# Kernel tuning notes

Measured on AMD Instinct MI355X. Metric: run time of the kernel, lower is better.

Reference implementation:

```python
import jax, jax.numpy as jnp
import numpy as np

B, S, D, K = 8, 4096, 256, 8192
BETA = 0.25


def setup_inputs() -> dict:
    key = jax.random.key(0)
    k1, k2 = jax.random.split(key)
    return {
        "z": jax.random.normal(k1, (B, S, D), dtype=jnp.float32),
        "embed": jax.random.normal(k2, (K, D), dtype=jnp.float32),
    }


def reference(z, embed):
    # Inference-path VQ-EMA forward (EMA buffer updates are a no-grad side
    # effect only active in training mode; excluded from the pure reference).
    num_codes, dim = embed.shape
    z_flat = z.reshape(-1, dim)                      # [N, D]
    # squared-euclidean distances: ||z||^2 - 2 z.e^T + ||e||^2  -> [N, K]
    dist = ((z_flat * z_flat).sum(1, keepdims=True)
            - 2.0 * (z_flat @ embed.T)
            + (embed * embed).sum(1)[None, :])
    idx = jnp.argmin(dist, axis=1)                   # [N]
    z_q = embed[idx].reshape(z.shape)                # gather instead of onehot @ embed
    # commitment loss: beta * mse(stop_grad(z_q), z)
    loss = BETA * jnp.mean(jnp.square(jax.lax.stop_gradient(z_q) - z))
    # straight-through estimator
    z_q_st = z + jax.lax.stop_gradient(z_q - z)
    # perplexity from code usage histogram (scatter-add instead of onehot.mean)
    counts = jnp.zeros((num_codes,), dtype=z.dtype).at[idx].add(1.0)
    avg_probs = counts / idx.shape[0]
    perplexity = jnp.exp(-jnp.sum(avg_probs * jnp.log(avg_probs + 1e-12)))
    return z_q_st, loss, perplexity, idx.reshape(z.shape[:-1])
```

## Files before the change

kernel.cpp:

```cpp
#include <hip/hip_runtime.h>
#include <stdint.h>
#include <math.h>

#define NROWS 32768
#define DIM   256
#define KCODES 8192
#define BETA  0.25f
#define CSPLIT 4
#define RSPLIT 16
#define NELEM 8388608
#define TAU 0.09375f

typedef float f32x4 __attribute__((ext_vector_type(4)));
typedef _Float16 v8h __attribute__((ext_vector_type(8)));
typedef unsigned short us4 __attribute__((ext_vector_type(4)));

__device__ inline unsigned int split1(float x) {
    _Float16 hf = (_Float16)x;
    _Float16 lf = (_Float16)(x - (float)hf);
    unsigned int h = __builtin_bit_cast(unsigned short, hf);
    unsigned int l = __builtin_bit_cast(unsigned short, lf);
    return h | (l << 16);
}

__device__ inline void gload_lds16(const void* g, void* l) {
    __builtin_amdgcn_global_load_lds(
        (const __attribute__((address_space(1))) void*)g,
        (__attribute__((address_space(3))) void*)l,
        16, 0, 0);
}

__device__ inline unsigned int fkey(float f) {
    unsigned int b = __float_as_uint(f);
    return (b & 0x80000000u) ? ~b : (b | 0x80000000u);
}

__global__ void prep_all(const float* __restrict__ z,
                         const float* __restrict__ e,
                         unsigned short* __restrict__ zhi,
                         unsigned short* __restrict__ zlo,
                         unsigned short* __restrict__ ehi,
                         unsigned short* __restrict__ elo,
                         float* __restrict__ enrm,
                         float* __restrict__ counts,
                         float* __restrict__ lossAcc,
                         int* __restrict__ flagcnt) {
    if (blockIdx.x < 8192) {
        int t = blockIdx.x * 256 + threadIdx.x;
        float4 v = reinterpret_cast<const float4*>(z)[t];
        unsigned int p0 = split1(v.x);
        unsigned int p1 = split1(v.y);
        unsigned int p2 = split1(v.z);
        unsigned int p3 = split1(v.w);
        us4 h, l;
        h[0] = (unsigned short)p0; l[0] = (unsigned short)(p0 >> 16);
        h[1] = (unsigned short)p1; l[1] = (unsigned short)(p1 >> 16);
        h[2] = (unsigned short)p2; l[2] = (unsigned short)(p2 >> 16);
        h[3] = (unsigned short)p3; l[3] = (unsigned short)(p3 >> 16);
        reinterpret_cast<us4*>(zhi)[t] = h;
        reinterpret_cast<us4*>(zlo)[t] = l;
    } else {
        int row = blockIdx.x - 8192;
        int d = threadIdx.x;
        float x = e[(size_t)row * DIM + d];
        unsigned int p = split1(x);
        ehi[(size_t)row * DIM + d] = (unsigned short)p;
        elo[(size_t)row * DIM + d] = (unsigned short)(p >> 16);
        float sq = x * x;
        #pragma unroll
        for (int off = 32; off; off >>= 1) sq += __shfl_down(sq, off);
        __shared__ float ps[4];
        if ((threadIdx.x & 63) == 0) ps[threadIdx.x >> 6] = sq;
        __syncthreads();
        if (threadIdx.x == 0) {
            enrm[row] = 0.5f * (ps[0] + ps[1] + ps[2] + ps[3]);
            counts[row] = 0.f;
            if (row == 0) { *lossAcc = 0.f; *flagcnt = 0; }
        }
    }
}

__launch_bounds__(256, 2)
__global__ void gemm_hi(const unsigned short* __restrict__ zhi,
                        const unsigned short* __restrict__ ehi,
                        const float* __restrict__ enrm,
                        float* __restrict__ pval1,
                        int* __restrict__ pcol1,
                        float* __restrict__ pval2) {
    __shared__ __align__(16) unsigned short As[128 * 64];
    __shared__ __align__(16) unsigned short Bs[128 * 64];
    __shared__ float rv[2][128];
    __shared__ int   rc[2][128];
    __shared__ float rv2[2][128];

    const int tid = threadIdx.x;
    const int w = tid >> 6, l = tid & 63;
    const int lx = l & 15, quad = l >> 4;
    const int wm = w >> 1, wn = w & 1;
    const int arow_base = blockIdx.x * 128;
    const int cs = blockIdx.y;
    const int cbase_cs = cs * (KCODES / CSPLIT);

    float runv[16], runv2[16];
    int runc[16];
    #pragma unroll
    for (int s = 0; s < 16; ++s) {
        runv[s] = 3.0e38f; runv2[s] = 3.0e38f; runc[s] = 0x7fffffff;
    }

    const int st_row8 = l >> 3;
    const int st_g = (((l & 7) ^ (l >> 3)) * 8);
    const int fr_lx7 = lx & 7;

    for (int nt = 0; nt < (KCODES / CSPLIT) / 128; ++nt) {
        const int colbase = cbase_cs + nt * 128;
        f32x4 acc[4][4];
        #pragma unroll
        for (int mi = 0; mi < 4; ++mi)
            #pragma unroll
            for (int ni = 0; ni < 4; ++ni) {
                f32x4 zz = {0.f, 0.f, 0.f, 0.f};
                acc[mi][ni] = zz;
            }

        for (int bk = 0; bk < 4; ++bk) {
            const int ao = bk * 64;
            __syncthreads();
            #pragma unroll
            for (int j = 0; j < 4; ++j) {
                const int r = w * 32 + j * 8 + st_row8;
                gload_lds16(zhi + (size_t)(arow_base + r) * DIM + ao + st_g,
                            &As[(w * 32 + j * 8) * 64]);
                gload_lds16(ehi + (size_t)(colbase + r) * DIM + ao + st_g,
                            &Bs[(w * 32 + j * 8) * 64]);
            }
            __syncthreads();

            #pragma unroll
            for (int kc = 0; kc < 2; ++kc) {
                const int gsw = ((kc * 4 + quad) ^ fr_lx7) * 8;
                v8h af[4], bfr[4];
                #pragma unroll
                for (int mi = 0; mi < 4; ++mi)
                    af[mi] = *(const v8h*)&As[(wm * 64 + mi * 16 + lx) * 64 + gsw];
                #pragma unroll
                for (int ni = 0; ni < 4; ++ni)
                    bfr[ni] = *(const v8h*)&Bs[(wn * 64 + ni * 16 + lx) * 64 + gsw];
                #pragma unroll
                for (int mi = 0; mi < 4; ++mi)
                    #pragma unroll
                    for (int ni = 0; ni < 4; ++ni)
                        acc[mi][ni] = __builtin_amdgcn_mfma_f32_16x16x32_f16(
                            af[mi], bfr[ni], acc[mi][ni], 0, 0, 0);
            }
        }

        #pragma unroll
        for (int ni = 0; ni < 4; ++ni) {
            const int col = colbase + wn * 64 + ni * 16 + lx;
            const float es = enrm[col];
            #pragma unroll
            for (int mi = 0; mi < 4; ++mi)
                #pragma unroll
                for (int r = 0; r < 4; ++r) {
                    const int s = mi * 4 + r;
                    float sv = es - acc[mi][ni][r];
                    bool lt = sv < runv[s];
                    runv2[s] = __builtin_amdgcn_fmed3f(sv, runv[s], runv2[s]);
                    runc[s] = lt ? col : runc[s];
                    runv[s] = fminf(runv[s], sv);
                }
        }
    }

    #pragma unroll
    for (int s = 0; s < 16; ++s) {
        float v1 = runv[s], v2 = runv2[s];
        int c1 = runc[s];
        #pragma unroll
        for (int m = 1; m < 16; m <<= 1) {
            float ov1 = __shfl_xor(v1, m);
            int oc1 = __shfl_xor(c1, m);
            float ov2 = __shfl_xor(v2, m);
            float mx = fmaxf(v1, ov1);
            v2 = fminf(fminf(v2, ov2), mx);
            bool take = (ov1 < v1) || (ov1 == v1 && oc1 < c1);
            v1 = take ? ov1 : v1;
            c1 = take ? oc1 : c1;
        }
        if (lx == 0) {
            const int mi = s >> 2, r = s & 3;
            const int rl = wm * 64 + mi * 16 + quad * 4 + r;
            rv[wn][rl] = v1; rc[wn][rl] = c1; rv2[wn][rl] = v2;
        }
    }
    __syncthreads();
    if (tid < 128) {
        float v1 = rv[0][tid], v2 = rv2[0][tid];
        int c1 = rc[0][tid];
        float ov1 = rv[1][tid], ov2 = rv2[1][tid];
        int oc1 = rc[1][tid];
        float mx = fmaxf(v1, ov1);
        v2 = fminf(fminf(v2, ov2), mx);
        bool take = (ov1 < v1) || (ov1 == v1 && oc1 < c1);
        v1 = take ? ov1 : v1;
        c1 = take ? oc1 : c1;
        const size_t row = (size_t)arow_base + tid;
        pval1[row * CSPLIT + cs] = v1;
        pcol1[row * CSPLIT + cs] = c1;
        pval2[row * CSPLIT + cs] = v2;
    }
}

__global__ void merge_flag(const float* __restrict__ pval1,
                           const int* __restrict__ pcol1,
                           const float* __restrict__ pval2,
                           int* __restrict__ colidx,
                           float* __restrict__ out_idx,
                           int* __restrict__ flagcnt,
                           int* __restrict__ flaglist,
                           unsigned long long* __restrict__ rkey) {
    int row = blockIdx.x * blockDim.x + threadIdx.x;
    float v1 = pval1[row * CSPLIT], v2 = pval2[row * CSPLIT];
    int c1 = pcol1[row * CSPLIT];
    #pragma unroll
    for (int cs = 1; cs < CSPLIT; ++cs) {
        float ov1 = pval1[row * CSPLIT + cs], ov2 = pval2[row * CSPLIT + cs];
        int oc1 = pcol1[row * CSPLIT + cs];
        float mx = fmaxf(v1, ov1);
        v2 = fminf(fminf(v2, ov2), mx);
        if (ov1 < v1 || (ov1 == v1 && oc1 < c1)) { v1 = ov1; c1 = oc1; }
    }
    out_idx[row] = (float)c1;
    if (v2 - v1 < TAU) {
        int slot = atomicAdd(flagcnt, 1);
        flaglist[slot] = row;
        rkey[slot] = ~0ull;
        colidx[row] = -(slot + 1);
    } else {
        colidx[row] = c1;
    }
}

__launch_bounds__(256, 2)
__global__ void rescue_gemm(const unsigned short* __restrict__ zhi,
                            const unsigned short* __restrict__ zlo,
                            const unsigned short* __restrict__ ehi,
                            const unsigned short* __restrict__ elo,
                            const float* __restrict__ enrm,
                            const int* __restrict__ flagcnt,
                            const int* __restrict__ flaglist,
                            unsigned long long* __restrict__ rkey) {
    __shared__ __align__(16) unsigned short As[128 * 64];
    __shared__ __align__(16) unsigned short Bs[128 * 64];
    __shared__ float rv[2][128];
    __shared__ int   rc[2][128];

    const int count = *flagcnt;
    const int tid = threadIdx.x;
    const int w = tid >> 6, l = tid & 63;
    const int lx = l & 15, quad = l >> 4;
    const int wm = w >> 1, wn = w & 1;
    const int cs = blockIdx.y;
    const int cbase_cs = cs * (KCODES / RSPLIT);

    const int st_row8 = l >> 3;
    const int st_g = (((l & 7) ^ (l >> 3)) * 8);
    const int fr_lx7 = lx & 7;

    for (int tb = blockIdx.x * 128; tb < count; tb += 32 * 128) {
        int arowj[4];
        #pragma unroll
        for (int j = 0; j < 4; ++j) {
            int li = tb + w * 32 + j * 8 + st_row8;
            arowj[j] = (li < count) ? flaglist[li] : 0;
        }

        float runv[16];
        int runc[16];
        #pragma unroll
        for (int s = 0; s < 16; ++s) { runv[s] = 3.0e38f; runc[s] = 0x7fffffff; }

        for (int nt = 0; nt < (KCODES / RSPLIT) / 128; ++nt) {
            const int colbase = cbase_cs + nt * 128;
            f32x4 acc[4][4];
            #pragma unroll
            for (int mi = 0; mi < 4; ++mi)
                #pragma unroll
                for (int ni = 0; ni < 4; ++ni) {
                    f32x4 zz = {0.f, 0.f, 0.f, 0.f};
                    acc[mi][ni] = zz;
                }

            #pragma unroll
            for (int seg = 0; seg < 3; ++seg) {
                const unsigned short* za = (seg == 2) ? zlo : zhi;
                const unsigned short* eb = (seg == 1) ? elo : ehi;
                for (int bk = 0; bk < 4; ++bk) {
                    const int ao = bk * 64;
                    __syncthreads();
                    #pragma unroll
                    for (int j = 0; j < 4; ++j) {
                        const int r = w * 32 + j * 8 + st_row8;
                        gload_lds16(za + (size_t)arowj[j] * DIM + ao + st_g,
                                    &As[(w * 32 + j * 8) * 64]);
                        gload_lds16(eb + (size_t)(colbase + r) * DIM + ao + st_g,
                                    &Bs[(w * 32 + j * 8) * 64]);
                    }
                    __syncthreads();
                    #pragma unroll
                    for (int kc = 0; kc < 2; ++kc) {
                        const int gsw = ((kc * 4 + quad) ^ fr_lx7) * 8;
                        v8h af[4], bfr[4];
                        #pragma unroll
                        for (int mi = 0; mi < 4; ++mi)
                            af[mi] = *(const v8h*)&As[(wm * 64 + mi * 16 + lx) * 64 + gsw];
                        #pragma unroll
                        for (int ni = 0; ni < 4; ++ni)
                            bfr[ni] = *(const v8h*)&Bs[(wn * 64 + ni * 16 + lx) * 64 + gsw];
                        #pragma unroll
                        for (int mi = 0; mi < 4; ++mi)
                            #pragma unroll
                            for (int ni = 0; ni < 4; ++ni)
                                acc[mi][ni] = __builtin_amdgcn_mfma_f32_16x16x32_f16(
                                    af[mi], bfr[ni], acc[mi][ni], 0, 0, 0);
                    }
                }
            }

            #pragma unroll
            for (int ni = 0; ni < 4; ++ni) {
                const int col = colbase + wn * 64 + ni * 16 + lx;
                const float es = enrm[col];
                #pragma unroll
                for (int mi = 0; mi < 4; ++mi)
                    #pragma unroll
                    for (int r = 0; r < 4; ++r) {
                        float sv = es - acc[mi][ni][r];
                        const int s = mi * 4 + r;
                        if (sv < runv[s]) { runv[s] = sv; runc[s] = col; }
                    }
            }
        }

        #pragma unroll
        for (int s = 0; s < 16; ++s) {
            float v = runv[s]; int c = runc[s];
            #pragma unroll
            for (int m = 1; m < 16; m <<= 1) {
                float ov = __shfl_xor(v, m);
                int oc = __shfl_xor(c, m);
                if (ov < v || (ov == v && oc < c)) { v = ov; c = oc; }
            }
            if (lx == 0) {
                const int mi = s >> 2, r = s & 3;
                const int rl = wm * 64 + mi * 16 + quad * 4 + r;
                rv[wn][rl] = v; rc[wn][rl] = c;
            }
        }
        __syncthreads();
        if (tid < 128) {
            float v0 = rv[0][tid]; int c0 = rc[0][tid];
            float v1 = rv[1][tid]; int c1 = rc[1][tid];
            if (v1 < v0 || (v1 == v0 && c1 < c0)) { v0 = v1; c0 = c1; }
            const int li = tb + tid;
            if (li < count) {
                unsigned long long key =
                    ((unsigned long long)fkey(v0) << 32) | (unsigned int)c0;
                atomicMin(&rkey[li], key);
            }
        }
        __syncthreads();
    }
}

__global__ void fused_out(const int* __restrict__ colidx,
                          const unsigned long long* __restrict__ rkey,
                          const float* __restrict__ z,
                          const float* __restrict__ embed,
                          float* __restrict__ out_zq,
                          float* __restrict__ out_idx,
                          float* __restrict__ counts,
                          float* __restrict__ lossAcc) {
    __shared__ int cidx[16];
    const int tid = threadIdx.x;
    if (tid < 16) {
        const int row = blockIdx.x * 16 + tid;
        int c = colidx[row];
        if (c < 0) {
            c = (int)(unsigned int)(rkey[-c - 1] & 0x1FFFull);
            out_idx[row] = (float)c;
        }
        cidx[tid] = c;
        atomicAdd(&counts[c], 1.0f);
    }
    __syncthreads();
    const int d = tid;
    float ls = 0.f;
    #pragma unroll 4
    for (int i = 0; i < 16; ++i) {
        const int row = blockIdx.x * 16 + i;
        const int c = cidx[i];
        const float zv = z[(size_t)row * DIM + d];
        const float ev = embed[(size_t)c * DIM + d];
        const float diff = ev - zv;
        out_zq[(size_t)row * DIM + d] = zv + diff;
        ls += diff * diff;
    }
    #pragma unroll
    for (int off = 32; off; off >>= 1) ls += __shfl_down(ls, off);
    __shared__ float ps[4];
    if ((tid & 63) == 0) ps[tid >> 6] = ls;
    __syncthreads();
    if (tid == 0) atomicAdd(lossAcc, ps[0] + ps[1] + ps[2] + ps[3]);
}

__global__ void finalize(const float* __restrict__ counts,
                         const float* __restrict__ lossAcc,
                         float* __restrict__ out_loss,
                         float* __restrict__ out_perp) {
    float h = 0.f;
    for (int k = threadIdx.x; k < KCODES; k += 256) {
        float p = counts[k] * (1.0f / (float)NROWS);
        h += p * logf(p + 1e-12f);
    }
    #pragma unroll
    for (int off = 32; off; off >>= 1) h += __shfl_down(h, off);
    __shared__ float ps[4];
    if ((threadIdx.x & 63) == 0) ps[threadIdx.x >> 6] = h;
    __syncthreads();
    if (threadIdx.x == 0) {
        *out_perp = expf(-(ps[0] + ps[1] + ps[2] + ps[3]));
        *out_loss = BETA * lossAcc[0] / (float)NELEM;
    }
}

extern "C" void kernel_launch(void* const* d_in, const int* in_sizes, int n_in,
                              void* d_out, int out_size, void* d_ws, size_t ws_size,
                              hipStream_t stream) {
    const float* z = (const float*)d_in[0];
    const float* embed = (const float*)d_in[1];
    char* ws = (char*)d_ws;

    unsigned short* zhi = (unsigned short*)(ws + 0);
    unsigned short* zlo = (unsigned short*)(ws + 16777216);
    unsigned short* ehi = (unsigned short*)(ws + 33554432);
    unsigned short* elo = (unsigned short*)(ws + 37748736);
    float* enrm    = (float*)(ws + 41943040);
    float* pval1   = (float*)(ws + 41975808);
    int*   pcol1   = (int*)  (ws + 42500096);
    float* pval2   = (float*)(ws + 43024384);
    int*   colidx  = (int*)  (ws + 43548672);
    float* counts  = (float*)(ws + 43679744);
    float* lossAcc = (float*)(ws + 43712512);
    int*   flagcnt = (int*)  (ws + 43712516);
    int*   flaglist = (int*) (ws + 43712520);
    unsigned long long* rkey = (unsigned long long*)(ws + 43843592);

    float* out = (float*)d_out;
    float* out_zq   = out;
    float* out_loss = out + 8388608;
    float* out_perp = out + 8388609;
    float* out_idx  = out + 8388610;

    prep_all<<<16384, 256, 0, stream>>>(z, embed, zhi, zlo, ehi, elo, enrm,
                                        counts, lossAcc, flagcnt);
    gemm_hi<<<dim3(NROWS / 128, CSPLIT), 256, 0, stream>>>(
        zhi, ehi, enrm, pval1, pcol1, pval2);
    merge_flag<<<NROWS / 256, 256, 0, stream>>>(
        pval1, pcol1, pval2, colidx, out_idx, flagcnt, flaglist, rkey);
    rescue_gemm<<<dim3(32, RSPLIT), 256, 0, stream>>>(
        zhi, zlo, ehi, elo, enrm, flagcnt, flaglist, rkey);
    fused_out<<<NROWS / 16, 256, 0, stream>>>(colidx, rkey, z, embed,
                                              out_zq, out_idx, counts, lossAcc);
    finalize<<<1, 256, 0, stream>>>(counts, lossAcc, out_loss, out_perp);
}
```

Measured before the change: 369.3 us.

## Fuse hi-precision GEMM with merge; keep A in registers and ring-buffer B tiles

Replaces the codebook-split GEMM plus separate merge kernel with one 512-thread kernel per 128-row block. Each block scans all 8192 codes, holds the z fragments in registers for the whole run, and keeps code norms in LDS. B tiles stream through a 4-stage LDS ring with async global-to-LDS loads, explicit vmcnt waits and priority hints. The top-2 merge and flagging happen in-kernel, which removes the partial-result buffers and one launch. The trade-off is a grid of only 256 blocks, which may reduce parallelism on the device, plus high register pressure from the 32 A fragments.

```diff
diff --git a/kernel.cpp b/kernel.cpp
--- a/kernel.cpp
+++ b/kernel.cpp
@@ -6,7 +6,6 @@
 #define DIM   256
 #define KCODES 8192
 #define BETA  0.25f
-#define CSPLIT 4
 #define RSPLIT 16
 #define NELEM 8388608
 #define TAU 0.09375f
@@ -80,26 +79,51 @@
     }
 }
 
-__launch_bounds__(256, 2)
-__global__ void gemm_hi(const unsigned short* __restrict__ zhi,
-                        const unsigned short* __restrict__ ehi,
-                        const float* __restrict__ enrm,
-                        float* __restrict__ pval1,
-                        int* __restrict__ pcol1,
-                        float* __restrict__ pval2) {
-    __shared__ __align__(16) unsigned short As[128 * 64];
-    __shared__ __align__(16) unsigned short Bs[128 * 64];
-    __shared__ float rv[2][128];
-    __shared__ int   rc[2][128];
-    __shared__ float rv2[2][128];
+__launch_bounds__(512, 2)
+__global__ void gemm_hi_fused(const unsigned short* __restrict__ zhi,
+                              const unsigned short* __restrict__ ehi,
+                              const float* __restrict__ enrm,
+                              int* __restrict__ colidx,
+                              float* __restrict__ out_idx,
+                              int* __restrict__ flagcnt,
+                              int* __restrict__ flaglist,
+                              unsigned long long* __restrict__ rkey) {
+    __shared__ __align__(16) unsigned short Bs[4][128 * 64];
+    __shared__ float esL[KCODES];
+    __shared__ float rvv[4][128];
+    __shared__ float rv2s[4][128];
+    __shared__ int   rcc[4][128];
 
     const int tid = threadIdx.x;
     const int w = tid >> 6, l = tid & 63;
     const int lx = l & 15, quad = l >> 4;
-    const int wm = w >> 1, wn = w & 1;
+    const int wm = w >> 2, wn = w & 3;
     const int arow_base = blockIdx.x * 128;
-    const int cs = blockIdx.y;
-    const int cbase_cs = cs * (KCODES / CSPLIT);
+    const int st_g = ((l & 7) ^ (l >> 3)) * 8;
+    const int fr_lx7 = lx & 7;
+
+    v8h af[4][8];
+    #pragma unroll
+    for (int mi = 0; mi < 4; ++mi) {
+        const unsigned short* ap =
+            zhi + (size_t)(arow_base + wm * 64 + mi * 16 + lx) * DIM + quad * 8;
+        #pragma unroll
+        for (int ks = 0; ks < 8; ++ks)
+            af[mi][ks] = *(const v8h*)(ap + ks * 32);
+    }
+
+    #pragma unroll
+    for (int j = 0; j < 4; ++j)
+        gload_lds16(enrm + (j * 8 + w) * 256 + l * 4, &esL[(j * 8 + w) * 256]);
+
+#define STAGE(BUF, SN, AO) do {                                               \
+        const unsigned short* _s0 =                                           \
+            ehi + (size_t)((SN) * 128 + (tid >> 3)) * DIM + (AO) + st_g;      \
+        gload_lds16(_s0, &Bs[BUF][(w * 8) * 64]);                             \
+        gload_lds16(_s0 + (size_t)64 * DIM, &Bs[BUF][(64 + w * 8) * 64]);     \
+    } while (0)
+
+    STAGE(0, 0, 0); STAGE(1, 0, 64); STAGE(2, 0, 128);
 
     float runv[16], runv2[16];
     int runc[16];
@@ -108,70 +132,63 @@
         runv[s] = 3.0e38f; runv2[s] = 3.0e38f; runc[s] = 0x7fffffff;
     }
 
-    const int st_row8 = l >> 3;
-    const int st_g = (((l & 7) ^ (l >> 3)) * 8);
-    const int fr_lx7 = lx & 7;
-
-    for (int nt = 0; nt < (KCODES / CSPLIT) / 128; ++nt) {
-        const int colbase = cbase_cs + nt * 128;
-        f32x4 acc[4][4];
+    for (int nt = 0; nt < 64; ++nt) {
+        f32x4 acc[4][2];
         #pragma unroll
         for (int mi = 0; mi < 4; ++mi)
             #pragma unroll
-            for (int ni = 0; ni < 4; ++ni) {
+            for (int ni = 0; ni < 2; ++ni) {
                 f32x4 zz = {0.f, 0.f, 0.f, 0.f};
                 acc[mi][ni] = zz;
             }
 
+        #pragma unroll
         for (int bk = 0; bk < 4; ++bk) {
-            const int ao = bk * 64;
-            __syncthreads();
-            #pragma unroll
-            for (int j = 0; j < 4; ++j) {
-                const int r = w * 32 + j * 8 + st_row8;
-                gload_lds16(zhi + (size_t)(arow_base + r) * DIM + ao + st_g,
-                            &As[(w * 32 + j * 8) * 64]);
-                gload_lds16(ehi + (size_t)(colbase + r) * DIM + ao + st_g,
-                            &Bs[(w * 32 + j * 8) * 64]);
-            }
-            __syncthreads();
-
+            const int sn = (bk == 0) ? nt : ((nt + 1) & 63);
+            STAGE((bk + 3) & 3, sn, ((bk + 3) & 3) * 64);
+            asm volatile("s_waitcnt vmcnt(6)" ::: "memory");
+            __builtin_amdgcn_s_barrier();
+            asm volatile("" ::: "memory");
+
+            __builtin_amdgcn_s_setprio(1);
             #pragma unroll
             for (int kc = 0; kc < 2; ++kc) {
                 const int gsw = ((kc * 4 + quad) ^ fr_lx7) * 8;
-                v8h af[4], bfr[4];
+                v8h b0 = *(const v8h*)&Bs[bk][(wn * 32 + lx) * 64 + gsw];
+                v8h b1 = *(const v8h*)&Bs[bk][(wn * 32 + 16 + lx) * 64 + gsw];
                 #pragma unroll
-                for (int mi = 0; mi < 4; ++mi)
-                    af[mi] = *(const v8h*)&As[(wm * 64 + mi * 16 + lx) * 64 + gsw];
-                #pragma unroll
-                for (int ni = 0; ni < 4; ++ni)
-                    bfr[ni] = *(const v8h*)&Bs[(wn * 64 + ni * 16 + lx) * 64 + gsw];
-                #pragma unroll
-                for (int mi = 0; mi < 4; ++mi)
-                    #pragma unroll
-                    for (int ni = 0; ni < 4; ++ni)
-                        acc[mi][ni] = __builtin_amdgcn_mfma_f32_16x16x32_f16(
-                            af[mi], bfr[ni], acc[mi][ni], 0, 0, 0);
-            }
-        }
-
-        #pragma unroll
-        for (int ni = 0; ni < 4; ++ni) {
-            const int col = colbase + wn * 64 + ni * 16 + lx;
-            const float es = enrm[col];
+                for (int mi = 0; mi < 4; ++mi) {
+                    acc[mi][0] = __builtin_amdgcn_mfma_f32_16x16x32_f16(
+                        af[mi][bk * 2 + kc], b0, acc[mi][0], 0, 0, 0);
+                    acc[mi][1] = __builtin_amdgcn_mfma_f32_16x16x32_f16(
+                        af[mi][bk * 2 + kc], b1, acc[mi][1], 0, 0, 0);
+                }
+            }
+            __builtin_amdgcn_s_setprio(0);
+
+            asm volatile("" ::: "memory");
+            __builtin_amdgcn_s_barrier();
+        }
+
+        const int cb = nt * 128 + wn * 32 + lx;
+        #pragma unroll
+        for (int ni = 0; ni < 2; ++ni) {
+            const int col = cb + ni * 16;
+            const float es = esL[col];
             #pragma unroll
             for (int mi = 0; mi < 4; ++mi)
                 #pragma unroll
                 for (int r = 0; r < 4; ++r) {
                     const int s = mi * 4 + r;
-                    float sv = es - acc[mi][ni][r];
-                    bool lt = sv < runv[s];
+                    const float sv = es - acc[mi][ni][r];
+                    const bool lt = sv < runv[s];
                     runv2[s] = __builtin_amdgcn_fmed3f(sv, runv[s], runv2[s]);
                     runc[s] = lt ? col : runc[s];
                     runv[s] = fminf(runv[s], sv);
                 }
         }
     }
+#undef STAGE
 
     #pragma unroll
     for (int s = 0; s < 16; ++s) {
@@ -189,56 +206,34 @@
             c1 = take ? oc1 : c1;
         }
         if (lx == 0) {
-            const int mi = s >> 2, r = s & 3;
-            const int rl = wm * 64 + mi * 16 + quad * 4 + r;
-            rv[wn][rl] = v1; rc[wn][rl] = c1; rv2[wn][rl] = v2;
+            const int rl = wm * 64 + (s >> 2) * 16 + quad * 4 + (s & 3);
+            rvv[wn][rl] = v1; rcc[wn][rl] = c1; rv2s[wn][rl] = v2;
         }
     }
     __syncthreads();
     if (tid < 128) {
-        float v1 = rv[0][tid], v2 = rv2[0][tid];
-        int c1 = rc[0][tid];
-        float ov1 = rv[1][tid], ov2 = rv2[1][tid];
-        int oc1 = rc[1][tid];
-        float mx = fmaxf(v1, ov1);
-        v2 = fminf(fminf(v2, ov2), mx);
-        bool take = (ov1 < v1) || (ov1 == v1 && oc1 < c1);
-        v1 = take ? ov1 : v1;
-        c1 = take ? oc1 : c1;
-        const size_t row = (size_t)arow_base + tid;
-        pval1[row * CSPLIT + cs] = v1;
-        pcol1[row * CSPLIT + cs] = c1;
-        pval2[row * CSPLIT + cs] = v2;
-    }
-}
-
-__global__ void merge_flag(const float* __restrict__ pval1,
-                           const int* __restrict__ pcol1,
-                           const float* __restrict__ pval2,
-                           int* __restrict__ colidx,
-                           float* __restrict__ out_idx,
-                           int* __restrict__ flagcnt,
-                           int* __restrict__ flaglist,
-                           unsigned long long* __restrict__ rkey) {
-    int row = blockIdx.x * blockDim.x + threadIdx.x;
-    float v1 = pval1[row * CSPLIT], v2 = pval2[row * CSPLIT];
-    int c1 = pcol1[row * CSPLIT];
-    #pragma unroll
-    for (int cs = 1; cs < CSPLIT; ++cs) {
-        float ov1 = pval1[row * CSPLIT + cs], ov2 = pval2[row * CSPLIT + cs];
-        int oc1 = pcol1[row * CSPLIT + cs];
-        float mx = fmaxf(v1, ov1);
-        v2 = fminf(fminf(v2, ov2), mx);
-        if (ov1 < v1 || (ov1 == v1 && oc1 < c1)) { v1 = ov1; c1 = oc1; }
-    }
-    out_idx[row] = (float)c1;
-    if (v2 - v1 < TAU) {
-        int slot = atomicAdd(flagcnt, 1);
-        flaglist[slot] = row;
-        rkey[slot] = ~0ull;
-        colidx[row] = -(slot + 1);
-    } else {
-        colidx[row] = c1;
+        float v1 = rvv[0][tid], v2 = rv2s[0][tid];
+        int c1 = rcc[0][tid];
+        #pragma unroll
+        for (int q = 1; q < 4; ++q) {
+            float ov1 = rvv[q][tid], ov2 = rv2s[q][tid];
+            int oc1 = rcc[q][tid];
+            float mx = fmaxf(v1, ov1);
+            v2 = fminf(fminf(v2, ov2), mx);
+            bool take = (ov1 < v1) || (ov1 == v1 && oc1 < c1);
+            v1 = take ? ov1 : v1;
+            c1 = take ? oc1 : c1;
+        }
+        const int row = arow_base + tid;
+        out_idx[row] = (float)c1;
+        if (v2 - v1 < TAU) {
+            int slot = atomicAdd(flagcnt, 1);
+            flaglist[slot] = row;
+            rkey[slot] = ~0ull;
+            colidx[row] = -(slot + 1);
+        } else {
+            colidx[row] = c1;
+        }
     }
 }
 
@@ -447,9 +442,6 @@
     unsigned short* ehi = (unsigned short*)(ws + 33554432);
     unsigned short* elo = (unsigned short*)(ws + 37748736);
     float* enrm    = (float*)(ws + 41943040);
-    float* pval1   = (float*)(ws + 41975808);
-    int*   pcol1   = (int*)  (ws + 42500096);
-    float* pval2   = (float*)(ws + 43024384);
     int*   colidx  = (int*)  (ws + 43548672);
     float* counts  = (float*)(ws + 43679744);
     float* lossAcc = (float*)(ws + 43712512);
@@ -465,10 +457,8 @@
 
     prep_all<<<16384, 256, 0, stream>>>(z, embed, zhi, zlo, ehi, elo, enrm,
                                         counts, lossAcc, flagcnt);
-    gemm_hi<<<dim3(NROWS / 128, CSPLIT), 256, 0, stream>>>(
-        zhi, ehi, enrm, pval1, pcol1, pval2);
-    merge_flag<<<NROWS / 256, 256, 0, stream>>>(
-        pval1, pcol1, pval2, colidx, out_idx, flagcnt, flaglist, rkey);
+    gemm_hi_fused<<<NROWS / 128, 512, 0, stream>>>(
+        zhi, ehi, enrm, colidx, out_idx, flagcnt, flaglist, rkey);
     rescue_gemm<<<dim3(32, RSPLIT), 256, 0, stream>>>(
         zhi, zlo, ehi, elo, enrm, flagcnt, flaglist, rkey);
     fused_out<<<NROWS / 16, 256, 0, stream>>>(colidx, rkey, z, embed,
```

After: 344.8 us. -6.6%, faster.
